# Kernel tuning notes

Measured on AMD Instinct MI355X. Metric: run time of the kernel, lower is better.

Reference implementation:

```python
import jax, jax.numpy as jnp
import numpy as np

N_TOKENS = 524288
N_FEATURES = 128
N_MODELS = 16
N_LAYERS = 2


def setup_inputs() -> dict:
    key = jax.random.key(0)
    kx, kw, kb = jax.random.split(key, 3)
    x = jax.random.normal(kx, (N_TOKENS, N_FEATURES), dtype=jnp.float32)
    # per-expert, per-layer Linear weights in torch layout [out, in]
    scale = 1.0 / np.sqrt(N_FEATURES)
    W = jax.random.normal(kw, (N_MODELS, N_LAYERS, N_FEATURES, N_FEATURES), dtype=jnp.float32) * scale
    b = jax.random.normal(kb, (N_MODELS, N_LAYERS, N_FEATURES), dtype=jnp.float32) * scale
    return {"x": x, "W": W, "b": b}


def reference(x, W, b):
    # x: [N, F]; W: [M, L, F_out, F_in]; b: [M, L, F_out]
    # slices = M equal contiguous partitions of the token dim; each slice runs
    # through its own Linear+ReLU stack and is scattered back (here: reshape).
    M, L, Fo, Fi = W.shape
    xs = x.reshape(M, -1, Fi)  # [M, N/M, F] gathered slices
    for l in range(L):  # small fixed depth loop
        xs = jax.nn.relu(jnp.einsum('mnf,mgf->mng', xs, W[:, l]) + b[:, l][:, None, :])
    return xs.reshape(x.shape[0], Fo)
```

## Files before the change

### kernel.cpp

```cpp
#include <hip/hip_runtime.h>


#define NF    128
#define NM    16
#define NTOK  524288
#define TPM   (NTOK / NM)
#define BM    128
#define TILES 8
#define BLKPM ((TPM / BM) / TILES)
#define WPAD  136

typedef __attribute__((ext_vector_type(8))) short bf16x8;
typedef __attribute__((ext_vector_type(4))) short bf16x4v;
typedef __attribute__((ext_vector_type(4))) float f32x4;
typedef unsigned int u32;

__device__ __forceinline__ unsigned short f2bf(float f) {
    union { float f; unsigned u; } v; v.f = f;
    unsigned r = v.u + 0x7FFFu + ((v.u >> 16) & 1u);
    return (unsigned short)(r >> 16);
}

__device__ alignas(16) unsigned short g_Wf[NM * 2 * NF * NF];

__global__ __launch_bounds__(256) void convw_kernel(const float* __restrict__ W) {
    const int idx  = blockIdx.x * 256 + threadIdx.x;
    const int lane = idx & 63;
    const int fid  = (idx >> 6) & 31;
    const int ml   = idx >> 11;
    const int row  = (fid >> 2) * 16 + (lane & 15);
    const int col  = (fid & 3) * 32 + (lane >> 4) * 8;
    const float* s = W + ((size_t)ml * NF + row) * NF + col;
    float4 a = *(const float4*)s;
    float4 c = *(const float4*)(s + 4);
    unsigned short* d = &g_Wf[(size_t)idx * 8];
    d[0] = f2bf(a.x); d[1] = f2bf(a.y); d[2] = f2bf(a.z); d[3] = f2bf(a.w);
    d[4] = f2bf(c.x); d[5] = f2bf(c.y); d[6] = f2bf(c.z); d[7] = f2bf(c.w);
}

__device__ __forceinline__ void load_lds16(const unsigned short* g, unsigned short* l) {
    __builtin_amdgcn_global_load_lds(
        (const __attribute__((address_space(1))) u32*)g,
        (__attribute__((address_space(3))) u32*)l, 16, 0, 0);
}

__global__ __launch_bounds__(512, 2) void mlp16_kernel(
        const float* __restrict__ x, const float* __restrict__ b,
        float* __restrict__ out) {
    __shared__ alignas(16) unsigned short sW0[NF * NF];
    __shared__ alignas(16) unsigned short sW1[NF * NF];
    __shared__ alignas(16) unsigned short sY[BM * WPAD];
    __shared__ alignas(16) float sB[2 * NF];

    const int t    = threadIdx.x;
    const int w    = t >> 6;
    const int lane = t & 63;
    const int ln   = lane & 15;
    const int q    = lane >> 4;

    const int m  = blockIdx.x / BLKPM;
    const int tg = blockIdx.x % BLKPM;

    if (t < 2 * NF) sB[t] = b[m * 2 * NF + t];

    const unsigned short* wsrc = g_Wf + (size_t)m * 2 * NF * NF;
    #pragma unroll
    for (int i = 0; i < 4; ++i) {
        const int fid = w * 4 + i;
        load_lds16(wsrc + (size_t)(fid * 64 + lane) * 8, &sW0[fid * 512]);
        load_lds16(wsrc + NF * NF + (size_t)(fid * 64 + lane) * 8, &sW1[fid * 512]);
    }

    const size_t tok0 = (size_t)m * TPM + (size_t)tg * (TILES * BM);
    const float* xrow = x + (tok0 + (size_t)(w * 16 + ln)) * NF;
    float*       orow = out + (tok0 + (size_t)(w * 16 + ln)) * NF;
    unsigned short*       syw = &sY[(w * 16 + ln) * WPAD];
    const unsigned short* syr = syw;

    float4 xa[8];
    #pragma unroll
    for (int kt = 0; kt < 4; ++kt) {
        xa[2 * kt]     = *(const float4*)(xrow + kt * 32 + q * 8);
        xa[2 * kt + 1] = *(const float4*)(xrow + kt * 32 + q * 8 + 4);
    }

    __syncthreads();

    for (int i = 0; i < TILES; ++i) {
        bf16x8 xb[4];
        #pragma unroll
        for (int kt = 0; kt < 4; ++kt) {
            const float4 a0 = xa[2 * kt], a1 = xa[2 * kt + 1];
            bf16x8 v;
            v[0] = (short)f2bf(a0.x); v[1] = (short)f2bf(a0.y);
            v[2] = (short)f2bf(a0.z); v[3] = (short)f2bf(a0.w);
            v[4] = (short)f2bf(a1.x); v[5] = (short)f2bf(a1.y);
            v[6] = (short)f2bf(a1.z); v[7] = (short)f2bf(a1.w);
            xb[kt] = v;
        }

        if (i + 1 < TILES) {
            const float* p = xrow + (size_t)(i + 1) * (BM * NF);
            #pragma unroll
            for (int kt = 0; kt < 4; ++kt) {
                xa[2 * kt]     = *(const float4*)(p + kt * 32 + q * 8);
                xa[2 * kt + 1] = *(const float4*)(p + kt * 32 + q * 8 + 4);
            }
        }

        f32x4 acc[8];
        #pragma unroll
        for (int gt = 0; gt < 8; ++gt) acc[gt] = *(const f32x4*)&sB[gt * 16 + q * 4];
        #pragma unroll
        for (int kt = 0; kt < 4; ++kt) {
            #pragma unroll
            for (int gt = 0; gt < 8; ++gt) {
                bf16x8 wf = *(const bf16x8*)&sW0[((gt * 4 + kt) * 64 + lane) * 8];
                acc[gt] = __builtin_amdgcn_mfma_f32_16x16x32_bf16(wf, xb[kt], acc[gt], 0, 0, 0);
            }
        }

        #pragma unroll
        for (int gt = 0; gt < 8; ++gt) {
            bf16x4v yv;
            #pragma unroll
            for (int r = 0; r < 4; ++r) {
                float vv = acc[gt][r];
                vv = vv > 0.f ? vv : 0.f;
                yv[r] = (short)f2bf(vv);
            }
            *(bf16x4v*)&syw[gt * 16 + q * 4] = yv;
        }
        asm volatile("" ::: "memory");

        f32x4 acc2[8];
        #pragma unroll
        for (int gt = 0; gt < 8; ++gt) acc2[gt] = *(const f32x4*)&sB[NF + gt * 16 + q * 4];
        #pragma unroll
        for (int kt = 0; kt < 4; ++kt) {
            const bf16x8 yb = *(const bf16x8*)(syr + kt * 32 + q * 8);
            #pragma unroll
            for (int gt = 0; gt < 8; ++gt) {
                bf16x8 wf = *(const bf16x8*)&sW1[((gt * 4 + kt) * 64 + lane) * 8];
                acc2[gt] = __builtin_amdgcn_mfma_f32_16x16x32_bf16(wf, yb, acc2[gt], 0, 0, 0);
            }
        }
        asm volatile("" ::: "memory");

        float* op = orow + (size_t)i * (BM * NF);
        #pragma unroll
        for (int gt = 0; gt < 8; ++gt) {
            float4 o;
            float v0 = acc2[gt][0]; o.x = v0 > 0.f ? v0 : 0.f;
            float v1 = acc2[gt][1]; o.y = v1 > 0.f ? v1 : 0.f;
            float v2 = acc2[gt][2]; o.z = v2 > 0.f ? v2 : 0.f;
            float v3 = acc2[gt][3]; o.w = v3 > 0.f ? v3 : 0.f;
            *(float4*)(op + gt * 16 + q * 4) = o;
        }
    }
}

extern "C" void kernel_launch(void* const* d_in, const int* in_sizes, int n_in,
                              void* d_out, int out_size, void* d_ws, size_t ws_size,
                              hipStream_t stream) {
    const float* x = (const float*)d_in[0];
    const float* W = (const float*)d_in[1];
    const float* b = (const float*)d_in[2];
    float* out = (float*)d_out;
    convw_kernel<<<dim3(256), dim3(256), 0, stream>>>(W);
    mlp16_kernel<<<dim3(NM * BLKPM), dim3(512), 0, stream>>>(x, b, out);
}
```

Baseline: 448.7 us.

## Keep layer-1 activations in registers by permuting layer-2 weight fragment layout

Drops the LDS staging buffer for the intermediate activations. Layer-1 MFMA outputs are fed straight into layer 2 as operands of 16x16x16 bf16 MFMAs, and the layer-2 weights are stored in an interleaved layout so the fragments line up with the accumulator register layout. This removes the LDS write and read round-trip and frees LDS, so launch bounds are raised to allow 4 blocks per CU. The cost is twice as many, smaller MFMA instructions for layer 2 and heavier register pressure at the higher occupancy target.

After: 874.1 us. 94.8% more time.

```diff
diff --git a/kernel.cpp b/kernel.cpp
--- a/kernel.cpp
+++ b/kernel.cpp
@@ -8,7 +8,6 @@
 #define BM    128
 #define TILES 8
 #define BLKPM ((TPM / BM) / TILES)
-#define WPAD  136
 
 typedef __attribute__((ext_vector_type(8))) short bf16x8;
 typedef __attribute__((ext_vector_type(4))) short bf16x4v;
@@ -26,13 +25,16 @@
 __global__ __launch_bounds__(256) void convw_kernel(const float* __restrict__ W) {
     const int idx  = blockIdx.x * 256 + threadIdx.x;
     const int lane = idx & 63;
+    const int q    = lane >> 4;
     const int fid  = (idx >> 6) & 31;
     const int ml   = idx >> 11;
     const int row  = (fid >> 2) * 16 + (lane & 15);
-    const int col  = (fid & 3) * 32 + (lane >> 4) * 8;
-    const float* s = W + ((size_t)ml * NF + row) * NF + col;
-    float4 a = *(const float4*)s;
-    float4 c = *(const float4*)(s + 4);
+    const float* base = W + ((size_t)ml * NF + row) * NF;
+    int c0, c1;
+    if (ml & 1) { c0 = (fid & 3) * 32 + q * 4; c1 = c0 + 16; }
+    else        { c0 = (fid & 3) * 32 + q * 8; c1 = c0 + 4;  }
+    float4 a = *(const float4*)(base + c0);
+    float4 c = *(const float4*)(base + c1);
     unsigned short* d = &g_Wf[(size_t)idx * 8];
     d[0] = f2bf(a.x); d[1] = f2bf(a.y); d[2] = f2bf(a.z); d[3] = f2bf(a.w);
     d[4] = f2bf(c.x); d[5] = f2bf(c.y); d[6] = f2bf(c.z); d[7] = f2bf(c.w);
@@ -44,12 +46,11 @@
         (__attribute__((address_space(3))) u32*)l, 16, 0, 0);
 }
 
-__global__ __launch_bounds__(512, 2) void mlp16_kernel(
+__global__ __launch_bounds__(512, 4) void mlp16_kernel(
         const float* __restrict__ x, const float* __restrict__ b,
         float* __restrict__ out) {
     __shared__ alignas(16) unsigned short sW0[NF * NF];
     __shared__ alignas(16) unsigned short sW1[NF * NF];
-    __shared__ alignas(16) unsigned short sY[BM * WPAD];
     __shared__ alignas(16) float sB[2 * NF];
 
     const int t    = threadIdx.x;
@@ -74,8 +75,6 @@
     const size_t tok0 = (size_t)m * TPM + (size_t)tg * (TILES * BM);
     const float* xrow = x + (tok0 + (size_t)(w * 16 + ln)) * NF;
     float*       orow = out + (tok0 + (size_t)(w * 16 + ln)) * NF;
-    unsigned short*       syw = &sY[(w * 16 + ln) * WPAD];
-    const unsigned short* syr = syw;
 
     float4 xa[8];
     #pragma unroll
@@ -120,32 +119,33 @@
             }
         }
 
+        bf16x4v yb[8];
         #pragma unroll
-        for (int gt = 0; gt < 8; ++gt) {
+        for (int gtk = 0; gtk < 8; ++gtk) {
             bf16x4v yv;
             #pragma unroll
             for (int r = 0; r < 4; ++r) {
-                float vv = acc[gt][r];
+                float vv = acc[gtk][r];
                 vv = vv > 0.f ? vv : 0.f;
                 yv[r] = (short)f2bf(vv);
             }
-            *(bf16x4v*)&syw[gt * 16 + q * 4] = yv;
+            yb[gtk] = yv;
         }
-        asm volatile("" ::: "memory");
 
         f32x4 acc2[8];
         #pragma unroll
         for (int gt = 0; gt < 8; ++gt) acc2[gt] = *(const f32x4*)&sB[NF + gt * 16 + q * 4];
         #pragma unroll
-        for (int kt = 0; kt < 4; ++kt) {
-            const bf16x8 yb = *(const bf16x8*)(syr + kt * 32 + q * 8);
+        for (int ktp = 0; ktp < 4; ++ktp) {
             #pragma unroll
-            for (int gt = 0; gt < 8; ++gt) {
-                bf16x8 wf = *(const bf16x8*)&sW1[((gt * 4 + kt) * 64 + lane) * 8];
-                acc2[gt] = __builtin_amdgcn_mfma_f32_16x16x32_bf16(wf, yb, acc2[gt], 0, 0, 0);
+            for (int gt2 = 0; gt2 < 8; ++gt2) {
+                bf16x8 wf = *(const bf16x8*)&sW1[((gt2 * 4 + ktp) * 64 + lane) * 8];
+                bf16x4v lo = __builtin_shufflevector(wf, wf, 0, 1, 2, 3);
+                bf16x4v hi = __builtin_shufflevector(wf, wf, 4, 5, 6, 7);
+                acc2[gt2] = __builtin_amdgcn_mfma_f32_16x16x16bf16_1k(lo, yb[2 * ktp],     acc2[gt2], 0, 0, 0);
+                acc2[gt2] = __builtin_amdgcn_mfma_f32_16x16x16bf16_1k(hi, yb[2 * ktp + 1], acc2[gt2], 0, 0, 0);
             }
         }
-        asm volatile("" ::: "memory");
 
         float* op = orow + (size_t)i * (BM * NF);
         #pragma unroll
```
